# Performance work log

Measured on AMD Instinct MI355X. Metric: run time of the kernel, lower is better.

Reference implementation:

```python
import jax, jax.numpy as jnp
import numpy as np
from jax import lax

B, N, W, L, H = 8, 1024, 1024, 12, 16
EPS = 1e-5


def setup_inputs() -> dict:
    key = jax.random.key(0)
    ks = jax.random.split(key, 14)
    std = 0.25 / np.sqrt(W)  # init_scale * sqrt(1/width)
    inp = {
        "x": jax.random.normal(ks[0], (B, N, W), dtype=jnp.float32),
        # stacked per-layer params, leading dim L
        "ln1_g": jnp.ones((L, W), jnp.float32),
        "ln1_b": jnp.zeros((L, W), jnp.float32),
        "w_qkv": jax.random.normal(ks[1], (L, W, 3 * W), jnp.float32) * std,
        "b_qkv": jnp.zeros((L, 3 * W), jnp.float32),
        "w_o":   jax.random.normal(ks[2], (L, W, W), jnp.float32) * std,
        "b_o":   jnp.zeros((L, W), jnp.float32),
        "ln2_g": jnp.ones((L, W), jnp.float32),
        "ln2_b": jnp.zeros((L, W), jnp.float32),
        "w_fc":  jax.random.normal(ks[3], (L, W, 4 * W), jnp.float32) * std,
        "b_fc":  jnp.zeros((L, 4 * W), jnp.float32),
        "w_pr":  jax.random.normal(ks[4], (L, 4 * W, W), jnp.float32) * std,
        "b_pr":  jnp.zeros((L, W), jnp.float32),
    }
    return inp


def _layernorm(x, g, b):
    mu = jnp.mean(x, axis=-1, keepdims=True)
    var = jnp.mean(jnp.square(x - mu), axis=-1, keepdims=True)
    return (x - mu) * lax.rsqrt(var + EPS) * g + b


def _attention(qkv, heads):
    # qkv: [B, N, 3W]; matches QKVMultiheadAttention exactly
    bs, n_ctx, width3 = qkv.shape
    attn_ch = width3 // heads // 3
    scale = 1.0 / np.sqrt(np.sqrt(attn_ch))
    qkv = qkv.reshape(bs, n_ctx, heads, 3 * attn_ch)
    q, k, v = jnp.split(qkv, 3, axis=-1)  # each [B,N,H,c]
    w = jnp.einsum("bthc,bshc->bhts", q * scale, k * scale)
    w = jax.nn.softmax(w.astype(jnp.float32), axis=-1).astype(qkv.dtype)
    out = jnp.einsum("bhts,bshc->bthc", w, v)
    return out.reshape(bs, n_ctx, heads * attn_ch)


def reference(x, ln1_g, ln1_b, w_qkv, b_qkv, w_o, b_o,
              ln2_g, ln2_b, w_fc, b_fc, w_pr, b_pr):
    params = (ln1_g, ln1_b, w_qkv, b_qkv, w_o, b_o,
              ln2_g, ln2_b, w_fc, b_fc, w_pr, b_pr)

    def step(h, p):
        (g1, bb1, wqkv, bqkv, wo, bo, g2, bb2, wfc, bfc, wpr, bpr) = p
        a = _layernorm(h, g1, bb1)
        a = jnp.einsum("bnw,wk->bnk", a, wqkv) + bqkv
        a = _attention(a, H)
        a = jnp.einsum("bnw,wk->bnk", a, wo) + bo
        h = h + a
        m = _layernorm(h, g2, bb2)
        m = jax.nn.gelu(jnp.einsum("bnw,wf->bnf", m, wfc) + bfc, approximate=False)
        m = jnp.einsum("bnf,fw->bnw", m, wpr) + bpr
        return h + m, None

    out, _ = lax.scan(step, x, params)
    return out
```

## Files before the change

### kernel.cpp

```cpp
#include <hip/hip_runtime.h>
#include <cstdint>
#include <cstddef>

#define WDIM 1024
#define BDIM 8
#define NDIM 1024
#define LDIM 12
#define HDIM 16
#define MROWS (BDIM * NDIM)

using bf16x8 = __attribute__((ext_vector_type(8))) __bf16;
using f32x4  = __attribute__((ext_vector_type(4))) float;
using u16x8  = __attribute__((ext_vector_type(8))) ushort;

static __device__ __forceinline__ f32x4 mfma16(bf16x8 a, bf16x8 b, f32x4 c) {
  return __builtin_amdgcn_mfma_f32_16x16x32_bf16(a, b, c, 0, 0, 0);
}

static __device__ __forceinline__ ushort f2bf(float f) {
  uint32_t u = __builtin_bit_cast(uint32_t, f);
  u = (u + 0x7FFFu + ((u >> 16) & 1u)) >> 16;
  return (ushort)u;
}

static __device__ __forceinline__ void g2lds16(const void* g, void* l) {
  __builtin_amdgcn_global_load_lds(
      (__attribute__((address_space(1))) void*)(g),
      (__attribute__((address_space(3))) void*)(l), 16, 0, 0);
}

__global__ __launch_bounds__(256) void ln_kernel(const float* __restrict__ h,
                                                 const float* __restrict__ g,
                                                 const float* __restrict__ b,
                                                 ushort* __restrict__ out) {
  const int row = blockIdx.x;
  const int tid = threadIdx.x;
  const float4 v = ((const float4*)(h + (size_t)row * WDIM))[tid];
  float s  = v.x + v.y + v.z + v.w;
  float s2 = v.x * v.x + v.y * v.y + v.z * v.z + v.w * v.w;
  for (int off = 32; off; off >>= 1) {
    s  += __shfl_xor(s, off);
    s2 += __shfl_xor(s2, off);
  }
  __shared__ float red[8];
  const int w = tid >> 6;
  if ((tid & 63) == 0) { red[w] = s; red[4 + w] = s2; }
  __syncthreads();
  s  = red[0] + red[1] + red[2] + red[3];
  s2 = red[4] + red[5] + red[6] + red[7];
  const float mu   = s * (1.0f / WDIM);
  const float var  = s2 * (1.0f / WDIM) - mu * mu;
  const float rstd = rsqrtf(var + 1e-5f);
  const float4 gv = ((const float4*)g)[tid];
  const float4 bv = ((const float4*)b)[tid];
  ushort4 o;
  o.x = f2bf((v.x - mu) * rstd * gv.x + bv.x);
  o.y = f2bf((v.y - mu) * rstd * gv.y + bv.y);
  o.z = f2bf((v.z - mu) * rstd * gv.z + bv.z);
  o.w = f2bf((v.w - mu) * rstd * gv.w + bv.w);
  ((ushort4*)(out + (size_t)row * WDIM))[tid] = o;
}

__global__ __launch_bounds__(256) void transpose_cvt(const float* __restrict__ in,
                                                     ushort* __restrict__ out,
                                                     int K, int N) {
  __shared__ float sm[32][33];
  const int n0 = blockIdx.x * 32, k0 = blockIdx.y * 32;
  const int tx = threadIdx.x, ty = threadIdx.y;
  #pragma unroll
  for (int j = 0; j < 4; ++j)
    sm[ty + j * 8][tx] = in[(size_t)(k0 + ty + j * 8) * N + n0 + tx];
  __syncthreads();
  #pragma unroll
  for (int j = 0; j < 4; ++j)
    out[(size_t)(n0 + ty + j * 8) * K + k0 + tx] = f2bf(sm[tx][ty + j * 8]);
}

__global__ __launch_bounds__(256) void v_transpose(const ushort* __restrict__ qkv,
                                                   ushort* __restrict__ vT) {
  const int nb = blockIdx.x, bh = blockIdx.y;
  const int b = bh >> 4, h = bh & 15;
  const int tid = threadIdx.x;
  __shared__ ushort smT[64 * 64];
  const int n0 = nb * 64;
  const size_t rowb = (size_t)b * NDIM;
  #pragma unroll
  for (int p = 0; p < 2; ++p) {
    const int n  = p * 32 + (tid >> 3);
    const int d0 = (tid & 7) * 8;
    const uint4 vv = *(const uint4*)(qkv + (rowb + n0 + n) * 3072 + h * 192 + 128 + d0);
    const ushort* e = (const ushort*)&vv;
    const int key = d0;
    #pragma unroll
    for (int j = 0; j < 8; ++j)
      smT[(d0 + j) * 64 + (n ^ key)] = e[j];
  }
  __syncthreads();
  #pragma unroll
  for (int p = 0; p < 2; ++p) {
    const int d  = p * 32 + (tid >> 3);
    const int nc = (tid & 7) * 8;
    const int key = (d >> 3) << 3;
    const uint4 ov = *(const uint4*)&smT[d * 64 + (nc ^ key)];
    *(uint4*)(vT + ((size_t)bh * 64 + d) * NDIM + n0 + nc) = ov;
  }
}

enum { EPI_BF16 = 0, EPI_RES = 1, EPI_GELU = 2 };

template <int EPI>
__global__ __launch_bounds__(256) void gemm_kernel(
    const ushort* __restrict__ A, const ushort* __restrict__ Bt,
    const float* __restrict__ bias, float* __restrict__ resid,
    ushort* __restrict__ outb, int M, int N, int K) {
  __shared__ ushort smA[2][128 * 32];
  __shared__ ushort smB[2][128 * 32];
  const int tid = threadIdx.x;
  const int w = tid >> 6, l = tid & 63;
  const int lr = l & 15, lg = l >> 4;
  const int wr = (w >> 1) * 64, wc = (w & 1) * 64;
  const int row0 = blockIdx.y * 128, col0 = blockIdx.x * 128;
  const int cr = l >> 2;
  const int ccol = (l & 3) * 8;
  f32x4 acc[4][4] = {};
  const int KT = K >> 5;

  auto stage = [&](int buf, int kt) {
    const int kb = kt << 5;
    #pragma unroll
    for (int j = 0; j < 2; ++j) {
      const int c = w * 2 + j;
      g2lds16(A  + (size_t)(row0 + c * 16 + cr) * K + kb + ccol, &smA[buf][c * 512]);
      g2lds16(Bt + (size_t)(col0 + c * 16 + cr) * K + kb + ccol, &smB[buf][c * 512]);
    }
  };

  stage(0, 0);
  int cur = 0;
  for (int kt = 0; kt < KT; ++kt) {
    __syncthreads();
    if (kt + 1 < KT) stage(cur ^ 1, kt + 1);
    bf16x8 af[4], bfr[4];
    #pragma unroll
    for (int t = 0; t < 4; ++t) {
      af[t]  = *(const bf16x8*)&smA[cur][(wr + t * 16 + lr) * 32 + lg * 8];
      bfr[t] = *(const bf16x8*)&smB[cur][(wc + t * 16 + lr) * 32 + lg * 8];
    }
    #pragma unroll
    for (int mt = 0; mt < 4; ++mt)
      #pragma unroll
      for (int nt = 0; nt < 4; ++nt)
        acc[mt][nt] = mfma16(af[mt], bfr[nt], acc[mt][nt]);
    cur ^= 1;
  }

  #pragma unroll
  for (int mt = 0; mt < 4; ++mt) {
    #pragma unroll
    for (int nt = 0; nt < 4; ++nt) {
      #pragma unroll
      for (int i = 0; i < 4; ++i) {
        const int r = row0 + wr + mt * 16 + lg * 4 + i;
        const int c = col0 + wc + nt * 16 + lr;
        float v = acc[mt][nt][i] + bias[c];
        if constexpr (EPI == EPI_RES) {
          resid[(size_t)r * N + c] += v;
        } else if constexpr (EPI == EPI_GELU) {
          const float gg = 0.5f * v * (1.0f + erff(v * 0.70710678118f));
          outb[(size_t)r * N + c] = f2bf(gg);
        } else {
          outb[(size_t)r * N + c] = f2bf(v);
        }
      }
    }
  }
}

__global__ __launch_bounds__(512) void attn_kernel(const ushort* __restrict__ qkv,
                                                   const ushort* __restrict__ vT,
                                                   ushort* __restrict__ out) {
  const int qb = blockIdx.x;
  const int bh = blockIdx.y;
  const int b = bh >> 4, h = bh & 15;
  const int tid = threadIdx.x;
  const int w = tid >> 6, l = tid & 63;
  const int lr = l & 15, lg = l >> 4;
  __shared__ ushort smK[2][64 * 64];
  __shared__ ushort smV[2][64 * 64];
  __shared__ ushort smP[8][16 * 64];
  const int q0 = qb * 128 + w * 16;
  const size_t rowb = (size_t)b * NDIM;
  const ushort* vhead = vT + (size_t)bh * 64 * NDIM;
  ushort* P = smP[w];

  const u16x8 ob = {0x3F80, 0x3F80, 0x3F80, 0x3F80, 0x3F80, 0x3F80, 0x3F80, 0x3F80};
  const bf16x8 onesv = __builtin_bit_cast(bf16x8, ob);

  const int srow = l >> 3;
  const int scol = ((l & 7) ^ srow) * 8;
  const ushort* kg = qkv + (rowb + w * 8 + srow) * 3072 + h * 192 + 64 + scol;
  const ushort* vg = vhead + (size_t)(w * 8 + srow) * NDIM + scol;

  auto stage = [&](int buf, int kb) {
    g2lds16(kg + (size_t)kb * 64 * 3072, &smK[buf][w * 512]);
    g2lds16(vg + kb * 64,                &smV[buf][w * 512]);
  };

  bf16x8 qf0, qf1;
  {
    const ushort* qp = qkv + (rowb + q0 + lr) * 3072 + h * 192;
    qf0 = *(const bf16x8*)(qp + lg * 8);
    qf1 = *(const bf16x8*)(qp + 32 + lg * 8);
  }
  f32x4 o[4] = {};
  f32x4 lacc = {0.f, 0.f, 0.f, 0.f};

  stage(0, 0);
  int cur = 0;
  for (int kb = 0; kb < NDIM / 64; ++kb) {
    __syncthreads();
    if (kb + 1 < NDIM / 64) stage(cur ^ 1, kb + 1);

    const int rs = lr & 7;
    f32x4 s[4];
    #pragma unroll
    for (int kt = 0; kt < 4; ++kt) {
      const ushort* krow = &smK[cur][(kt * 16 + lr) * 64];
      const bf16x8 kf0 = *(const bf16x8*)&krow[(lg ^ rs) * 8];
      const bf16x8 kf1 = *(const bf16x8*)&krow[((4 + lg) ^ rs) * 8];
      f32x4 z = {0.f, 0.f, 0.f, 0.f};
      s[kt] = mfma16(qf1, kf1, mfma16(qf0, kf0, z));
    }

    #pragma unroll
    for (int i = 0; i < 4; ++i) {
      const int row = lg * 4 + i;
      const int swz = (row & 7) << 3;
      ushort* pr = P + row * 64;
      pr[lr ^ swz]        = f2bf(__expf(s[0][i] * 0.125f));
      pr[(16 + lr) ^ swz] = f2bf(__expf(s[1][i] * 0.125f));
      pr[(32 + lr) ^ swz] = f2bf(__expf(s[2][i] * 0.125f));
      pr[(48 + lr) ^ swz] = f2bf(__expf(s[3][i] * 0.125f));
    }

    const int rswz = rs << 3;
    const bf16x8 pf0 = *(const bf16x8*)&P[lr * 64 + ((lg * 8) ^ rswz)];
    const bf16x8 pf1 = *(const bf16x8*)&P[lr * 64 + ((32 + lg * 8) ^ rswz)];
    lacc = mfma16(pf0, onesv, mfma16(pf1, onesv, lacc));
    #pragma unroll
    for (int dt = 0; dt < 4; ++dt) {
      const ushort* vrow = &smV[cur][(dt * 16 + lr) * 64];
      const bf16x8 vf0 = *(const bf16x8*)&vrow[(lg ^ rs) * 8];
      const bf16x8 vf1 = *(const bf16x8*)&vrow[((4 + lg) ^ rs) * 8];
      o[dt] = mfma16(pf0, vf0, mfma16(pf1, vf1, o[dt]));
    }
    cur ^= 1;
  }

  #pragma unroll
  for (int i = 0; i < 4; ++i) {
    const float inv = 1.0f / lacc[i];
    const size_t orow = (rowb + q0 + lg * 4 + i) * (size_t)WDIM;
    #pragma unroll
    for (int dt = 0; dt < 4; ++dt)
      out[orow + h * 64 + dt * 16 + lr] = f2bf(o[dt][i] * inv);
  }
}

extern "C" void kernel_launch(void* const* d_in, const int* in_sizes, int n_in,
                              void* d_out, int out_size, void* d_ws, size_t ws_size,
                              hipStream_t stream) {
  const float* x     = (const float*)d_in[0];
  const float* ln1_g = (const float*)d_in[1];
  const float* ln1_b = (const float*)d_in[2];
  const float* w_qkv = (const float*)d_in[3];
  const float* b_qkv = (const float*)d_in[4];
  const float* w_o   = (const float*)d_in[5];
  const float* b_o   = (const float*)d_in[6];
  const float* ln2_g = (const float*)d_in[7];
  const float* ln2_b = (const float*)d_in[8];
  const float* w_fc  = (const float*)d_in[9];
  const float* b_fc  = (const float*)d_in[10];
  const float* w_pr  = (const float*)d_in[11];
  const float* b_pr  = (const float*)d_in[12];

  float* hbuf = (float*)d_out;

  uint8_t* p = (uint8_t*)d_ws;
  ushort* wqkv_t = (ushort*)p; p += (size_t)3072 * 1024 * 2;
  ushort* wo_t   = (ushort*)p; p += (size_t)1024 * 1024 * 2;
  ushort* wfc_t  = (ushort*)p; p += (size_t)4096 * 1024 * 2;
  ushort* wpr_t  = (ushort*)p; p += (size_t)1024 * 4096 * 2;
  ushort* lnb    = (ushort*)p; p += (size_t)MROWS * 1024 * 2;
  ushort* qkvb   = (ushort*)p; p += (size_t)MROWS * 3072 * 2;
  ushort* attnb  = (ushort*)p; p += (size_t)MROWS * 1024 * 2;
  ushort* mlpb   = (ushort*)p; p += (size_t)MROWS * 4096 * 2;
  ushort* vTb    = (ushort*)p; p += (size_t)BDIM * HDIM * 64 * NDIM * 2;

  hipMemcpyAsync(hbuf, x, (size_t)MROWS * WDIM * sizeof(float),
                 hipMemcpyDeviceToDevice, stream);

  for (int l = 0; l < LDIM; ++l) {
    ln_kernel<<<MROWS, 256, 0, stream>>>(hbuf, ln1_g + l * 1024, ln1_b + l * 1024, lnb);
    transpose_cvt<<<dim3(3072 / 32, 1024 / 32), dim3(32, 8), 0, stream>>>(
        w_qkv + (size_t)l * 1024 * 3072, wqkv_t, 1024, 3072);
    gemm_kernel<EPI_BF16><<<dim3(24, 64), 256, 0, stream>>>(
        lnb, wqkv_t, b_qkv + (size_t)l * 3072, nullptr, qkvb, MROWS, 3072, 1024);
    v_transpose<<<dim3(16, 128), 256, 0, stream>>>(qkvb, vTb);
    attn_kernel<<<dim3(8, 128), 512, 0, stream>>>(qkvb, vTb, attnb);
    transpose_cvt<<<dim3(32, 32), dim3(32, 8), 0, stream>>>(
        w_o + (size_t)l * 1024 * 1024, wo_t, 1024, 1024);
    gemm_kernel<EPI_RES><<<dim3(8, 64), 256, 0, stream>>>(
        attnb, wo_t, b_o + (size_t)l * 1024, hbuf, nullptr, MROWS, 1024, 1024);
    ln_kernel<<<MROWS, 256, 0, stream>>>(hbuf, ln2_g + l * 1024, ln2_b + l * 1024, lnb);
    transpose_cvt<<<dim3(4096 / 32, 1024 / 32), dim3(32, 8), 0, stream>>>(
        w_fc + (size_t)l * 1024 * 4096, wfc_t, 1024, 4096);
    gemm_kernel<EPI_GELU><<<dim3(32, 64), 256, 0, stream>>>(
        lnb, wfc_t, b_fc + (size_t)l * 4096, nullptr, mlpb, MROWS, 4096, 1024);
    transpose_cvt<<<dim3(1024 / 32, 4096 / 32), dim3(32, 8), 0, stream>>>(
        w_pr + (size_t)l * 4096 * 1024, wpr_t, 4096, 1024);
    gemm_kernel<EPI_RES><<<dim3(8, 64), 256, 0, stream>>>(
        mlpb, wpr_t, b_pr + (size_t)l * 1024, hbuf, nullptr, MROWS, 1024, 4096);
  }
}
```

Before: 5.026 ms.

## Deepen GEMM K-tile to 64 with XOR-swizzled LDS, XCD block remap, MFMA priority

Raises the GEMM K step from 32 to 64, halving the number of barriers and K iterations, and doubles the LDS buffers. Global-to-LDS staging now writes an XOR-swizzled layout so fragment reads avoid bank conflicts. Block IDs are remapped so neighbouring tiles land on the same XCD for better L2 reuse, and s_setprio raises wave priority around the MFMA block. In exchange the kernel uses more LDS and registers, which may lower occupancy.

```diff
diff --git a/kernel.cpp b/kernel.cpp
--- a/kernel.cpp
+++ b/kernel.cpp
@@ -113,25 +113,32 @@
     const ushort* __restrict__ A, const ushort* __restrict__ Bt,
     const float* __restrict__ bias, float* __restrict__ resid,
     ushort* __restrict__ outb, int M, int N, int K) {
-  __shared__ ushort smA[2][128 * 32];
-  __shared__ ushort smB[2][128 * 32];
+  __shared__ ushort smA[2][128 * 64];
+  __shared__ ushort smB[2][128 * 64];
   const int tid = threadIdx.x;
   const int w = tid >> 6, l = tid & 63;
   const int lr = l & 15, lg = l >> 4;
   const int wr = (w >> 1) * 64, wc = (w & 1) * 64;
-  const int row0 = blockIdx.y * 128, col0 = blockIdx.x * 128;
-  const int cr = l >> 2;
-  const int ccol = (l & 3) * 8;
+
+  const int gx = gridDim.x;
+  const int nwg = gx * gridDim.y;
+  const int id0 = blockIdx.y * gx + blockIdx.x;
+  const int id = (id0 & 7) * (nwg >> 3) + (id0 >> 3);
+  const int row0 = (id / gx) * 128, col0 = (id % gx) * 128;
+
+  const int srow = tid >> 3;
+  const int sslot = tid & 7;
   f32x4 acc[4][4] = {};
-  const int KT = K >> 5;
+  const int KT = K >> 6;
 
   auto stage = [&](int buf, int kt) {
-    const int kb = kt << 5;
-    #pragma unroll
-    for (int j = 0; j < 2; ++j) {
-      const int c = w * 2 + j;
-      g2lds16(A  + (size_t)(row0 + c * 16 + cr) * K + kb + ccol, &smA[buf][c * 512]);
-      g2lds16(Bt + (size_t)(col0 + c * 16 + cr) * K + kb + ccol, &smB[buf][c * 512]);
+    const int kb = kt << 6;
+    #pragma unroll
+    for (int j = 0; j < 4; ++j) {
+      const int r = j * 32 + srow;
+      const int sc = ((sslot ^ (r & 7)) * 8);
+      g2lds16(A  + (size_t)(row0 + r) * K + kb + sc, &smA[buf][j * 2048 + w * 512]);
+      g2lds16(Bt + (size_t)(col0 + r) * K + kb + sc, &smB[buf][j * 2048 + w * 512]);
     }
   };
 
@@ -140,17 +147,26 @@
   for (int kt = 0; kt < KT; ++kt) {
     __syncthreads();
     if (kt + 1 < KT) stage(cur ^ 1, kt + 1);
-    bf16x8 af[4], bfr[4];
-    #pragma unroll
-    for (int t = 0; t < 4; ++t) {
-      af[t]  = *(const bf16x8*)&smA[cur][(wr + t * 16 + lr) * 32 + lg * 8];
-      bfr[t] = *(const bf16x8*)&smB[cur][(wc + t * 16 + lr) * 32 + lg * 8];
-    }
-    #pragma unroll
-    for (int mt = 0; mt < 4; ++mt)
+    bf16x8 af[2][4], bfr[2][4];
+    const int rs = lr & 7;
+    #pragma unroll
+    for (int kk = 0; kk < 2; ++kk) {
       #pragma unroll
-      for (int nt = 0; nt < 4; ++nt)
-        acc[mt][nt] = mfma16(af[mt], bfr[nt], acc[mt][nt]);
+      for (int t = 0; t < 4; ++t) {
+        const int k8 = (kk * 4 + lg) ^ rs;
+        af[kk][t]  = *(const bf16x8*)&smA[cur][(wr + t * 16 + lr) * 64 + k8 * 8];
+        bfr[kk][t] = *(const bf16x8*)&smB[cur][(wc + t * 16 + lr) * 64 + k8 * 8];
+      }
+    }
+    __builtin_amdgcn_s_setprio(1);
+    #pragma unroll
+    for (int kk = 0; kk < 2; ++kk)
+      #pragma unroll
+      for (int mt = 0; mt < 4; ++mt)
+        #pragma unroll
+        for (int nt = 0; nt < 4; ++nt)
+          acc[mt][nt] = mfma16(af[kk][mt], bfr[kk][nt], acc[mt][nt]);
+    __builtin_amdgcn_s_setprio(0);
     cur ^= 1;
   }
 
```

New measurement: 4.547 ms. 1.11x faster.
